# Performance work log

Hardware: AMD Instinct MI355X
Metric: run time of the kernel (lower is better)

Reference implementation:

```python
import jax, jax.numpy as jnp
import numpy as np

B, S, D_MODEL, N_HEADS, HIDDEN = 4, 2048, 1024, 16, 4096
D_HEAD = D_MODEL // N_HEADS
LN_EPS = 1e-5


def setup_inputs() -> dict:
    key = jax.random.key(0)
    ks = jax.random.split(key, 20)
    s = 0.02
    return {
        "X": jax.random.normal(ks[0], (B, S, D_MODEL), dtype=jnp.float32),
        # attention projections (stored [in, out]; y = x @ W + b)
        "Wq": jax.random.normal(ks[1], (D_MODEL, D_MODEL), dtype=jnp.float32) * s,
        "bq": jnp.zeros((D_MODEL,), jnp.float32),
        "Wk": jax.random.normal(ks[2], (D_MODEL, D_MODEL), dtype=jnp.float32) * s,
        "bk": jnp.zeros((D_MODEL,), jnp.float32),
        "Wv": jax.random.normal(ks[3], (D_MODEL, D_MODEL), dtype=jnp.float32) * s,
        "bv": jnp.zeros((D_MODEL,), jnp.float32),
        "Wo": jax.random.normal(ks[4], (D_MODEL, D_MODEL), dtype=jnp.float32) * s,
        "bo": jnp.zeros((D_MODEL,), jnp.float32),
        # layernorm 1
        "g1": jnp.ones((D_MODEL,), jnp.float32),
        "beta1": jnp.zeros((D_MODEL,), jnp.float32),
        # FFN
        "W1": jax.random.normal(ks[5], (D_MODEL, HIDDEN), dtype=jnp.float32) * s,
        "b1": jnp.zeros((HIDDEN,), jnp.float32),
        "W2": jax.random.normal(ks[6], (HIDDEN, D_MODEL), dtype=jnp.float32) * s,
        "b2": jnp.zeros((D_MODEL,), jnp.float32),
        # layernorm 2
        "g2": jnp.ones((D_MODEL,), jnp.float32),
        "beta2": jnp.zeros((D_MODEL,), jnp.float32),
    }


def _layer_norm(x, gamma, beta):
    mu = jnp.mean(x, axis=-1, keepdims=True)
    var = jnp.mean(jnp.square(x - mu), axis=-1, keepdims=True)
    return (x - mu) * jax.lax.rsqrt(var + LN_EPS) * gamma + beta


def reference(X, Wq, bq, Wk, bk, Wv, bv, Wo, bo, g1, beta1, W1, b1, W2, b2, g2, beta2):
    b, s, d = X.shape
    # multi-head attention (dropout is identity in eval mode)
    q = (X @ Wq + bq).reshape(b, s, N_HEADS, D_HEAD)
    k = (X @ Wk + bk).reshape(b, s, N_HEADS, D_HEAD)
    v = (X @ Wv + bv).reshape(b, s, N_HEADS, D_HEAD)
    scale = 1.0 / np.sqrt(D_HEAD).astype(np.float32)
    scores = jnp.einsum('bqhd,bkhd->bhqk', q, k) * scale
    attn = jax.nn.softmax(scores, axis=-1)
    ctx = jnp.einsum('bhqk,bkhd->bqhd', attn, v).reshape(b, s, d)
    attn_out = ctx @ Wo + bo
    # AddNorm 1
    Y = _layer_norm(X + attn_out, g1, beta1)
    # FFN
    ffn_out = jax.nn.relu(Y @ W1 + b1) @ W2 + b2
    # AddNorm 2
    return _layer_norm(Y + ffn_out, g2, beta2)
```

## Files before the change

kernel.cpp:

```cpp
#include <hip/hip_runtime.h>
#include <stdint.h>

typedef unsigned short u16;
typedef short bf16x8 __attribute__((ext_vector_type(8)));
typedef float f32x4 __attribute__((ext_vector_type(4)));
typedef u16 u16x4 __attribute__((ext_vector_type(4)));
typedef u16 u16x8 __attribute__((ext_vector_type(8)));

#define LOG2E 1.4426950408889634f
#define QSCALE (0.125f * LOG2E)

__device__ __forceinline__ u16 f2bf(float f) {
  union { float f; uint32_t u; } x; x.f = f;
  uint32_t r = x.u + 0x7fffu + ((x.u >> 16) & 1u);
  return (u16)(r >> 16);
}
__device__ __forceinline__ u16 f2bf_ru(float f) {
  union { float f; uint32_t u; } x; x.f = f;
  return (u16)((x.u + 0x8000u) >> 16);
}
__device__ __forceinline__ float bf2f(u16 h) {
  union { uint32_t u; float f; } x; x.u = ((uint32_t)h) << 16;
  return x.f;
}
__device__ __forceinline__ uint32_t cvtpk(float lo, float hi) {
  uint32_t r;
  asm("v_cvt_pk_bf16_f32 %0, %1, %2" : "=v"(r) : "v"(lo), "v"(hi));
  return r;
}
__device__ __forceinline__ int swz3(int row) { return (row ^ (row >> 3)) & 7; }

__device__ __forceinline__ void gload_lds16(const void* g, void* lds) {
  __builtin_amdgcn_global_load_lds(
      (const __attribute__((address_space(1))) void*)g,
      (__attribute__((address_space(3))) void*)lds, 16, 0, 0);
}

__global__ __launch_bounds__(256) void cast_bf16(const float* __restrict__ in,
                                                 u16* __restrict__ out, int n8) {
  int i = blockIdx.x * 256 + threadIdx.x;
  const int stride = gridDim.x * 256;
  for (; i < n8; i += stride) {
    const f32x4* p = (const f32x4*)in + (size_t)i * 2;
    f32x4 a = p[0], b = p[1];
    u16x8 o;
    o[0] = f2bf(a[0]); o[1] = f2bf(a[1]); o[2] = f2bf(a[2]); o[3] = f2bf(a[3]);
    o[4] = f2bf(b[0]); o[5] = f2bf(b[1]); o[6] = f2bf(b[2]); o[7] = f2bf(b[3]);
    ((u16x8*)out)[i] = o;
  }
}

__global__ __launch_bounds__(256) void concat3(const float* __restrict__ a,
                                               const float* __restrict__ b,
                                               const float* __restrict__ c,
                                               float* __restrict__ o) {
  int i = blockIdx.x * 256 + threadIdx.x;
  if (i < 3072)
    o[i] = i < 1024 ? a[i] * QSCALE : (i < 2048 ? b[i - 1024] : c[i - 2048]);
}

__global__ __launch_bounds__(256) void transpose_cast(const float* __restrict__ in,
                                                      u16* __restrict__ out, int R, int C,
                                                      float scale) {
  __shared__ float tile[32][33];
  const int bc = blockIdx.x * 32, br = blockIdx.y * 32;
  const int tx = threadIdx.x & 31, ty = threadIdx.x >> 5;
#pragma unroll
  for (int i = 0; i < 32; i += 8)
    tile[ty + i][tx] = in[(size_t)(br + ty + i) * C + bc + tx];
  __syncthreads();
#pragma unroll
  for (int i = 0; i < 32; i += 8)
    out[(size_t)(bc + ty + i) * R + br + tx] = f2bf(tile[tx][ty + i] * scale);
}

__global__ __launch_bounds__(256) void vtrans(const u16* __restrict__ QKV,
                                              u16* __restrict__ Vtg) {
  __shared__ u16 tl[64][65];
  const int t = threadIdx.x;
  const int sblk = blockIdx.x, h = blockIdx.y, b = blockIdx.z;
  const int s0 = sblk * 64;
  const size_t ibase = ((size_t)b * 2048) * 3072 + 2048 + h * 64;
#pragma unroll
  for (int i = 0; i < 2; i++) {
    const int idx = i * 256 + t;
    const int sl = idx >> 3, d0 = (idx & 7) * 8;
    bf16x8 v = *(const bf16x8*)&QKV[ibase + (size_t)(s0 + sl) * 3072 + d0];
#pragma unroll
    for (int e = 0; e < 8; e++) tl[d0 + e][sl] = (u16)v[e];
  }
  __syncthreads();
  const size_t ob = ((size_t)(b * 16 + h) * 64) * 2048;
#pragma unroll
  for (int i = 0; i < 2; i++) {
    const int idx = i * 256 + t;
    const int r = idx >> 3, c0 = (idx & 7) * 8;
    u16x8 o;
#pragma unroll
    for (int e = 0; e < 8; e++) o[e] = tl[r][c0 + e];
    *(u16x8*)&Vtg[ob + (size_t)r * 2048 + s0 + c0] = o;
  }
}

template <int RELU>
__global__ __launch_bounds__(256) void gemm_bt(const u16* __restrict__ A,
                                               const u16* __restrict__ BT,
                                               const float* __restrict__ bias,
                                               u16* __restrict__ Cb,
                                               int M, int N, int K) {
  constexpr int BM = 128, BN = 128, BK = 64;
  __shared__ u16 As[BM * BK];
  __shared__ u16 Bs[BN * BK];
  const int t = threadIdx.x;
  const int w = t >> 6, lane = t & 63;
  const int la = lane & 15, lb = lane >> 4;
  const int wr = w >> 1, wc = w & 1;
  const int m0 = blockIdx.y * BM, n0 = blockIdx.x * BN;

  f32x4 acc[4][4];
#pragma unroll
  for (int i = 0; i < 4; i++)
#pragma unroll
    for (int j = 0; j < 4; j++) acc[i][j] = (f32x4){0.f, 0.f, 0.f, 0.f};

  for (int kt = 0; kt < K; kt += BK) {
#pragma unroll
    for (int i = 0; i < 4; i++) {
      const int s = i * 256 + t;
      const int row = s >> 3, col = (s & 7) * 8;
      gload_lds16(A + (size_t)(m0 + row) * K + kt + col, &As[(i * 256 + w * 64) * 8]);
      gload_lds16(BT + (size_t)(n0 + row) * K + kt + col, &Bs[(i * 256 + w * 64) * 8]);
    }
    __syncthreads();
#pragma unroll
    for (int ks = 0; ks < 2; ks++) {
      bf16x8 af[4], bfr[4];
#pragma unroll
      for (int i = 0; i < 4; i++)
        af[i] = *(const bf16x8*)&As[(wr * 64 + i * 16 + la) * BK + ks * 32 + lb * 8];
#pragma unroll
      for (int j = 0; j < 4; j++)
        bfr[j] = *(const bf16x8*)&Bs[(wc * 64 + j * 16 + la) * BK + ks * 32 + lb * 8];
#pragma unroll
      for (int i = 0; i < 4; i++)
#pragma unroll
        for (int j = 0; j < 4; j++)
          acc[i][j] = __builtin_amdgcn_mfma_f32_16x16x32_bf16(af[i], bfr[j], acc[i][j], 0, 0, 0);
    }
    __syncthreads();
  }
#pragma unroll
  for (int i = 0; i < 4; i++) {
    const int r = m0 + wr * 64 + i * 16 + lb * 4;
#pragma unroll
    for (int j = 0; j < 4; j++) {
      const int c = n0 + wc * 64 + j * 16 + la;
      const float bv = bias[c];
#pragma unroll
      for (int rr = 0; rr < 4; rr++) {
        float v = acc[i][j][rr] + bv;
        if (RELU) v = fmaxf(v, 0.f);
        Cb[(size_t)(r + rr) * N + c] = f2bf(v);
      }
    }
  }
}

template <int RELU>
__global__ __launch_bounds__(512, 2) void gemm8p(const u16* __restrict__ A,
                                                 const u16* __restrict__ BT,
                                                 const float* __restrict__ bias,
                                                 u16* __restrict__ Cb,
                                                 int M, int N, int K, int nbx) {
  __shared__ u16 As[2][256 * 64];
  __shared__ u16 Bs[2][256 * 64];
  const int t = threadIdx.x;
  const int w = t >> 6, lane = t & 63;
  const int la = lane & 15, lb = lane >> 4;
  const int wr = w >> 2, wc = w & 3;
  int bid = (int)blockIdx.x;
  const int cpx = (int)gridDim.x >> 3;
  bid = (bid & 7) * cpx + (bid >> 3);
  const int m0 = (bid / nbx) * 256, n0 = (bid % nbx) * 256;
  const int NT = K >> 6;
  const int row64 = t >> 3;
  const int colp = ((t & 7) ^ swz3(row64)) << 3;

#define STG_A(buf, tile, q) \
  gload_lds16(A + (size_t)(m0 + (q)*64 + row64) * K + ((tile) << 6) + colp, \
              &As[buf][(q)*4096 + w * 512])
#define STG_B(buf, tile, q) \
  gload_lds16(BT + (size_t)(n0 + (q)*64 + row64) * K + ((tile) << 6) + colp, \
              &Bs[buf][(q)*4096 + w * 512])
#define LDA(dst, mf, ks) { const int r_ = wr * 128 + (mf)*16 + la; \
  dst = *(const bf16x8*)&As[cur][r_ * 64 + (((((ks) << 2) + lb) ^ swz3(r_)) << 3)]; }
#define LDB(dst, nf, ks) { const int r_ = wc * 64 + (nf)*16 + la; \
  dst = *(const bf16x8*)&Bs[cur][r_ * 64 + (((((ks) << 2) + lb) ^ swz3(r_)) << 3)]; }
#define MFMA16(mh, nh) \
  __builtin_amdgcn_s_setprio(1); \
  _Pragma("unroll") for (int ks = 0; ks < 2; ks++) \
  _Pragma("unroll") for (int i = 0; i < 4; i++) \
  _Pragma("unroll") for (int j = 0; j < 2; j++) \
    acc[(mh)*4 + i][(nh)*2 + j] = __builtin_amdgcn_mfma_f32_16x16x32_bf16( \
        af[i][ks], bfr[j][ks], acc[(mh)*4 + i][(nh)*2 + j], 0, 0, 0); \
  __builtin_amdgcn_s_setprio(0);
#define BAR1() __builtin_amdgcn_s_barrier(); \
  asm volatile("s_waitcnt lgkmcnt(0)" ::: "memory"); \
  __builtin_amdgcn_sched_barrier(0)

  f32x4 acc[8][4];
#pragma unroll
  for (int i = 0; i < 8; i++)
#pragma unroll
    for (int j = 0; j < 4; j++) acc[i][j] = (f32x4){0.f, 0.f, 0.f, 0.f};

  STG_A(0, 0, 0); STG_A(0, 0, 2);
  STG_B(0, 0, 0); STG_B(0, 0, 1); STG_B(0, 0, 2); STG_B(0, 0, 3);
  STG_A(0, 0, 1); STG_A(0, 0, 3);
  asm volatile("s_waitcnt vmcnt(2)" ::: "memory");
  __builtin_amdgcn_s_barrier();

  for (int tile = 0; tile < NT; ++tile) {
    const int cur = tile & 1, nxt = cur ^ 1;
    const bool hn = (tile + 1) < NT;
    bf16x8 af[4][2], bfr[2][2];
#pragma unroll
    for (int i = 0; i < 4; i++) { LDA(af[i][0], i, 0); LDA(af[i][1], i, 1); }
#pragma unroll
    for (int j = 0; j < 2; j++) { LDB(bfr[j][0], j, 0); LDB(bfr[j][1], j, 1); }
    if (hn) { STG_A(nxt, tile + 1, 0); STG_A(nxt, tile + 1, 2); }
    BAR1();
    MFMA16(0, 0);
    __builtin_amdgcn_s_barrier();
#pragma unroll
    for (int j = 0; j < 2; j++) { LDB(bfr[j][0], 2 + j, 0); LDB(bfr[j][1], 2 + j, 1); }
    if (hn) { STG_B(nxt, tile + 1, 0); STG_B(nxt, tile + 1, 1); }
    BAR1();
    MFMA16(0, 1);
    if (hn) { asm volatile("s_waitcnt vmcnt(4)" ::: "memory"); }
    else    { asm volatile("s_waitcnt vmcnt(0)" ::: "memory"); }
    __builtin_amdgcn_s_barrier();
#pragma unroll
    for (int i = 0; i < 4; i++) { LDA(af[i][0], 4 + i, 0); LDA(af[i][1], 4 + i, 1); }
#pragma unroll
    for (int j = 0; j < 2; j++) { LDB(bfr[j][0], j, 0); LDB(bfr[j][1], j, 1); }
    if (hn) { STG_B(nxt, tile + 1, 2); STG_B(nxt, tile + 1, 3); }
    BAR1();
    MFMA16(1, 0);
    __builtin_amdgcn_s_barrier();
#pragma unroll
    for (int j = 0; j < 2; j++) { LDB(bfr[j][0], 2 + j, 0); LDB(bfr[j][1], 2 + j, 1); }
    if (hn) { STG_A(nxt, tile + 1, 1); STG_A(nxt, tile + 1, 3); }
    BAR1();
    MFMA16(1, 1);
    if (hn) { asm volatile("s_waitcnt vmcnt(2)" ::: "memory"); }
    __builtin_amdgcn_s_barrier();
  }
#undef STG_A
#undef STG_B
#undef LDA
#undef LDB
#undef MFMA16
#undef BAR1

#pragma unroll
  for (int mf = 0; mf < 8; mf++) {
    const int r = m0 + wr * 128 + mf * 16 + lb * 4;
#pragma unroll
    for (int nf = 0; nf < 4; nf++) {
      const int c = n0 + wc * 64 + nf * 16 + la;
      const float bv = bias[c];
#pragma unroll
      for (int rr = 0; rr < 4; rr++) {
        float v = acc[mf][nf][rr] + bv;
        if (RELU) v = fmaxf(v, 0.f);
        Cb[(size_t)(r + rr) * N + c] = f2bf(v);
      }
    }
  }
}

__global__ __launch_bounds__(256) void attn_fwd(const u16* __restrict__ Qg,
                                                const u16* __restrict__ Kg,
                                                const u16* __restrict__ Vtg,
                                                u16* __restrict__ Og, int LDM) {
  constexpr int S = 2048, DMO = 1024;
  __shared__ u16 Ks[2][128 * 64];
  __shared__ u16 Vt[2][64 * 128];
  const int t = threadIdx.x, w = t >> 6, lane = t & 63;
  const int la = lane & 15, lb = lane >> 4;
  const int qb = blockIdx.x, h = blockIdx.y, b = blockIdx.z;
  const size_t base = ((size_t)b * S) * LDM + h * 64;
  const size_t vbase = ((size_t)(b * 16 + h) * 64) * 2048;
  const size_t obase = ((size_t)b * S) * DMO + h * 64;
  const int qrow0 = qb * 128 + w * 32;
  const int sl0 = la + 32 * (lb & 1), sl1 = sl0 + 16;
  const int jsel = lb >> 1;

#define ATT_STAGE(buf, kt_) { \
  _Pragma("unroll") for (int i = 0; i < 4; i++) { \
    const int s = i * 256 + t; const int r = s >> 3; const int cg = s & 7; \
    gload_lds16(Kg + base + (size_t)((kt_) + r) * LDM + ((cg ^ swz3(r)) << 3), \
                &Ks[buf][s * 8]); } \
  _Pragma("unroll") for (int i = 0; i < 4; i++) { \
    const int s = i * 256 + t; const int r = s >> 4; const int cg = s & 15; \
    gload_lds16(Vtg + vbase + (size_t)r * 2048 + (kt_) + ((cg ^ swz3(r)) << 3), \
                &Vt[buf][s * 8]); } }

  bf16x8 qf[2][2];
#pragma unroll
  for (int rf = 0; rf < 2; rf++)
#pragma unroll
    for (int ks = 0; ks < 2; ks++)
      qf[rf][ks] = *(const bf16x8*)&Qg[base + (size_t)(qrow0 + rf * 16 + la) * LDM + ks * 32 + lb * 8];

  f32x4 accO[2][4];
  float m[2], l[2];
#pragma unroll
  for (int i = 0; i < 2; i++) {
    m[i] = -1e30f; l[i] = 0.f;
#pragma unroll
    for (int j = 0; j < 4; j++) accO[i][j] = (f32x4){0.f, 0.f, 0.f, 0.f};
  }

  ATT_STAGE(0, 0);
  asm volatile("s_waitcnt vmcnt(0)" ::: "memory");
  __builtin_amdgcn_s_barrier();

  for (int kt2 = 0; kt2 < S / 128; ++kt2) {
    const int cur = kt2 & 1;
    if (kt2 + 1 < S / 128) ATT_STAGE(cur ^ 1, (kt2 + 1) * 128);

#pragma unroll
    for (int sub = 0; sub < 2; ++sub) {
      f32x4 st[4][2];
#pragma unroll
      for (int j = 0; j < 4; j++)
#pragma unroll
        for (int rf = 0; rf < 2; rf++) st[j][rf] = (f32x4){0.f, 0.f, 0.f, 0.f};
      __builtin_amdgcn_s_setprio(1);
#pragma unroll
      for (int ks = 0; ks < 2; ks++) {
        bf16x8 kf[4];
#pragma unroll
        for (int j = 0; j < 4; j++) {
          const int r = sub * 64 + j * 16 + la;
          kf[j] = *(const bf16x8*)&Ks[cur][r * 64 + ((((ks << 2) + lb) ^ swz3(r)) << 3)];
        }
#pragma unroll
        for (int j = 0; j < 4; j++)
#pragma unroll
          for (int rf = 0; rf < 2; rf++)
            st[j][rf] = __builtin_amdgcn_mfma_f32_16x16x32_bf16(kf[j], qf[rf][ks], st[j][rf], 0, 0, 0);
      }
      __builtin_amdgcn_s_setprio(0);

      bf16x8 pf[2][2];
#pragma unroll
      for (int rf = 0; rf < 2; rf++) {
        float rm = st[0][rf][0];
#pragma unroll
        for (int j = 0; j < 4; j++)
#pragma unroll
          for (int rr = 0; rr < 4; rr++) rm = fmaxf(rm, st[j][rf][rr]);
        if (__any(rm > m[rf] + 8.0f)) {
          rm = fmaxf(rm, __shfl_xor(rm, 16, 64));
          rm = fmaxf(rm, __shfl_xor(rm, 32, 64));
          const float mN = fmaxf(m[rf], rm);
          const float al = exp2f(m[rf] - mN);
          m[rf] = mN;
          l[rf] *= al;
#pragma unroll
          for (int rr = 0; rr < 4; rr++) {
            const float alr = __shfl(al, (lb << 2) + rr, 64);
#pragma unroll
            for (int cf = 0; cf < 4; cf++) accO[rf][cf][rr] *= alr;
          }
        }
        uint32_t wl[4], wh[4];
#pragma unroll
        for (int j = 0; j < 4; j++) {
          float p0 = exp2f(st[j][rf][0] - m[rf]);
          float p1 = exp2f(st[j][rf][1] - m[rf]);
          float p2 = exp2f(st[j][rf][2] - m[rf]);
          float p3 = exp2f(st[j][rf][3] - m[rf]);
          l[rf] += (p0 + p1) + (p2 + p3);
          wl[j] = cvtpk(p0, p1);
          wh[j] = cvtpk(p2, p3);
        }
#pragma unroll
        for (int ks = 0; ks < 2; ks++) {
          const int j0 = 2 * ks, j1 = 2 * ks + 1;
          uint32_t a0 = __shfl(wl[j0], sl0, 64), a1 = __shfl(wh[j0], sl0, 64);
          uint32_t a2 = __shfl(wl[j0], sl1, 64), a3 = __shfl(wh[j0], sl1, 64);
          uint32_t b0 = __shfl(wl[j1], sl0, 64), b1 = __shfl(wh[j1], sl0, 64);
          uint32_t b2 = __shfl(wl[j1], sl1, 64), b3 = __shfl(wh[j1], sl1, 64);
          union { uint32_t u[4]; bf16x8 v; } pk;
          pk.u[0] = jsel ? b0 : a0;
          pk.u[1] = jsel ? b1 : a1;
          pk.u[2] = jsel ? b2 : a2;
          pk.u[3] = jsel ? b3 : a3;
          pf[rf][ks] = pk.v;
        }
      }

      __builtin_amdgcn_s_setprio(1);
#pragma unroll
      for (int ks = 0; ks < 2; ks++) {
        bf16x8 vf[4];
#pragma unroll
        for (int cf = 0; cf < 4; cf++) {
          const int dr = cf * 16 + la;
          const int g = sub * 8 + ks * 4 + lb;
          vf[cf] = *(const bf16x8*)&Vt[cur][dr * 128 + ((g ^ swz3(dr)) << 3)];
        }
#pragma unroll
        for (int rf = 0; rf < 2; rf++)
#pragma unroll
          for (int cf = 0; cf < 4; cf++)
            accO[rf][cf] = __builtin_amdgcn_mfma_f32_16x16x32_bf16(pf[rf][ks], vf[cf], accO[rf][cf], 0, 0, 0);
      }
      __builtin_amdgcn_s_setprio(0);
    }

    asm volatile("s_waitcnt vmcnt(0)" ::: "memory");
    __builtin_amdgcn_s_barrier();
  }
#undef ATT_STAGE

#pragma unroll
  for (int rf = 0; rf < 2; rf++) {
    float l2 = l[rf];
    l2 += __shfl_xor(l2, 16, 64);
    l2 += __shfl_xor(l2, 32, 64);
    const float inv = 1.0f / l2;
#pragma unroll
    for (int rr = 0; rr < 4; rr++) {
      const float invr = __shfl(inv, (lb << 2) + rr, 64);
      const int r = qrow0 + rf * 16 + lb * 4 + rr;
#pragma unroll
      for (int cf = 0; cf < 4; cf++)
        Og[obase + (size_t)r * DMO + cf * 16 + la] = f2bf_ru(accO[rf][cf][rr] * invr);
    }
  }
}

template <int AF32, int OUTF32>
__global__ __launch_bounds__(256) void add_ln(const void* __restrict__ Ap,
                                              const u16* __restrict__ Bb,
                                              const float* __restrict__ g,
                                              const float* __restrict__ be,
                                              void* __restrict__ Yp) {
  constexpr int D = 1024;
  const int row = blockIdx.x, t = threadIdx.x;
  f32x4 a;
  if (AF32) {
    a = ((const f32x4*)((const float*)Ap + (size_t)row * D))[t];
  } else {
    u16x4 av = ((const u16x4*)((const u16*)Ap + (size_t)row * D))[t];
#pragma unroll
    for (int i = 0; i < 4; i++) a[i] = bf2f(av[i]);
  }
  u16x4 bv16 = ((const u16x4*)(Bb + (size_t)row * D))[t];
  f32x4 x;
#pragma unroll
  for (int i = 0; i < 4; i++) x[i] = a[i] + bf2f(bv16[i]);
  float s1 = x[0] + x[1] + x[2] + x[3];
  float s2 = x[0] * x[0] + x[1] * x[1] + x[2] * x[2] + x[3] * x[3];
#pragma unroll
  for (int off = 32; off > 0; off >>= 1) {
    s1 += __shfl_down(s1, off, 64);
    s2 += __shfl_down(s2, off, 64);
  }
  __shared__ float sm[8];
  const int w = t >> 6, lane = t & 63;
  if (lane == 0) { sm[w] = s1; sm[4 + w] = s2; }
  __syncthreads();
  s1 = sm[0] + sm[1] + sm[2] + sm[3];
  s2 = sm[4] + sm[5] + sm[6] + sm[7];
  const float mean = s1 * (1.0f / D);
  const float var = s2 * (1.0f / D) - mean * mean;
  const float rstd = rsqrtf(var + 1e-5f);
  const f32x4 gv = ((const f32x4*)g)[t];
  const f32x4 bv = ((const f32x4*)be)[t];
  f32x4 y;
#pragma unroll
  for (int i = 0; i < 4; i++) y[i] = (x[i] - mean) * rstd * gv[i] + bv[i];
  if (OUTF32) {
    ((f32x4*)((float*)Yp + (size_t)row * D))[t] = y;
  } else {
    u16x4 o;
#pragma unroll
    for (int i = 0; i < 4; i++) o[i] = f2bf(y[i]);
    ((u16x4*)((u16*)Yp + (size_t)row * D))[t] = o;
  }
}

extern "C" void kernel_launch(void* const* d_in, const int* in_sizes, int n_in,
                              void* d_out, int out_size, void* d_ws, size_t ws_size,
                              hipStream_t stream) {
  const float* X   = (const float*)d_in[0];
  const float* Wq  = (const float*)d_in[1];
  const float* bq  = (const float*)d_in[2];
  const float* Wk  = (const float*)d_in[3];
  const float* bk  = (const float*)d_in[4];
  const float* Wv  = (const float*)d_in[5];
  const float* bv  = (const float*)d_in[6];
  const float* Wo  = (const float*)d_in[7];
  const float* bo  = (const float*)d_in[8];
  const float* g1  = (const float*)d_in[9];
  const float* be1 = (const float*)d_in[10];
  const float* W1  = (const float*)d_in[11];
  const float* b1  = (const float*)d_in[12];
  const float* W2  = (const float*)d_in[13];
  const float* b2  = (const float*)d_in[14];
  const float* g2  = (const float*)d_in[15];
  const float* be2 = (const float*)d_in[16];

  const size_t MB = 1ull << 20;
  char* wsb = (char*)d_ws;
  u16*   WqkvT = (u16*)(wsb + 0 * MB);
  u16*   WoT   = (u16*)(wsb + 6 * MB);
  u16*   W1T   = (u16*)(wsb + 8 * MB);
  u16*   W2T   = (u16*)(wsb + 16 * MB);
  u16*   Xb    = (u16*)(wsb + 24 * MB);
  u16*   Ab    = (u16*)(wsb + 24 * MB);
  u16*   Fb    = (u16*)(wsb + 24 * MB);
  u16*   QKVb  = (u16*)(wsb + 40 * MB);
  u16*   Hb    = (u16*)(wsb + 40 * MB);
  float* bqkv  = (float*)(wsb + 88 * MB);
  u16*   Cx    = (u16*)(wsb + 88 * MB);
  u16*   Vt_g  = (u16*)(wsb + 104 * MB);
  u16*   Yb    = (u16*)(wsb + 104 * MB);
  (void)ws_size; (void)in_sizes; (void)n_in; (void)out_size;

  cast_bf16<<<2048, 256, 0, stream>>>(X, Xb, 8192 * 1024 / 8);
  concat3<<<12, 256, 0, stream>>>(bq, bk, bv, bqkv);
  transpose_cast<<<dim3(32, 32), 256, 0, stream>>>(Wq, WqkvT, 1024, 1024, QSCALE);
  transpose_cast<<<dim3(32, 32), 256, 0, stream>>>(Wk, WqkvT + 1024 * 1024, 1024, 1024, 1.0f);
  transpose_cast<<<dim3(32, 32), 256, 0, stream>>>(Wv, WqkvT + 2 * 1024 * 1024, 1024, 1024, 1.0f);
  transpose_cast<<<dim3(32, 32), 256, 0, stream>>>(Wo, WoT, 1024, 1024, 1.0f);
  transpose_cast<<<dim3(128, 32), 256, 0, stream>>>(W1, W1T, 1024, 4096, 1.0f);
  transpose_cast<<<dim3(32, 128), 256, 0, stream>>>(W2, W2T, 4096, 1024, 1.0f);

  gemm8p<0><<<32 * 12, 512, 0, stream>>>(Xb, WqkvT, bqkv, QKVb, 8192, 3072, 1024, 12);

  vtrans<<<dim3(32, 16, 4), 256, 0, stream>>>(QKVb, Vt_g);
  attn_fwd<<<dim3(16, 16, 4), 256, 0, stream>>>(QKVb, QKVb + 1024, Vt_g, Cx, 3072);

  gemm_bt<0><<<dim3(8, 64), 256, 0, stream>>>(Cx, WoT, bo, Ab, 8192, 1024, 1024);
  add_ln<1, 0><<<8192, 256, 0, stream>>>(X, Ab, g1, be1, Yb);
  gemm8p<1><<<32 * 16, 512, 0, stream>>>(Yb, W1T, b1, Hb, 8192, 4096, 1024, 16);
  gemm_bt<0><<<dim3(8, 64), 256, 0, stream>>>(Hb, W2T, b2, Fb, 8192, 1024, 4096);
  add_ln<0, 1><<<8192, 256, 0, stream>>>(Yb, Fb, g2, be2, d_out);
}
```

Measured before the change: 502.8 us.

## Replace simple GEMM with double-buffered swizzled 256x128 pipelined GEMM kernel

Replaces the single-buffered 128x128 gemm_bt with a new 512-thread, double-buffered 256x128-tile GEMM. It uses XOR-swizzled LDS, split-phase prefetch with vmcnt waits, setprio around the MFMA blocks, and a block-index remap for L2 locality. The new kernel serves the Wo and W2 projections and also the QKV projection in place of gemm8p with 256x256 tiles. The aim is to overlap global loads with MFMA work and remove LDS bank conflicts. In exchange, the smaller N tile on QKV lowers data reuse, and the 256x128 tiles give only 256 blocks for the N=1024 GEMMs, which may limit occupancy.

```diff
diff --git a/kernel.cpp b/kernel.cpp
--- a/kernel.cpp
+++ b/kernel.cpp
@@ -103,62 +103,99 @@
 }
 
 template <int RELU>
-__global__ __launch_bounds__(256) void gemm_bt(const u16* __restrict__ A,
-                                               const u16* __restrict__ BT,
-                                               const float* __restrict__ bias,
-                                               u16* __restrict__ Cb,
-                                               int M, int N, int K) {
-  constexpr int BM = 128, BN = 128, BK = 64;
-  __shared__ u16 As[BM * BK];
-  __shared__ u16 Bs[BN * BK];
+__global__ __launch_bounds__(512, 2) void gemm2p(const u16* __restrict__ A,
+                                                 const u16* __restrict__ BT,
+                                                 const float* __restrict__ bias,
+                                                 u16* __restrict__ Cb,
+                                                 int M, int N, int K, int nbx) {
+  __shared__ u16 As[2][256 * 64];
+  __shared__ u16 Bs[2][128 * 64];
   const int t = threadIdx.x;
   const int w = t >> 6, lane = t & 63;
   const int la = lane & 15, lb = lane >> 4;
-  const int wr = w >> 1, wc = w & 1;
-  const int m0 = blockIdx.y * BM, n0 = blockIdx.x * BN;
-
-  f32x4 acc[4][4];
-#pragma unroll
-  for (int i = 0; i < 4; i++)
-#pragma unroll
-    for (int j = 0; j < 4; j++) acc[i][j] = (f32x4){0.f, 0.f, 0.f, 0.f};
-
-  for (int kt = 0; kt < K; kt += BK) {
-#pragma unroll
-    for (int i = 0; i < 4; i++) {
-      const int s = i * 256 + t;
-      const int row = s >> 3, col = (s & 7) * 8;
-      gload_lds16(A + (size_t)(m0 + row) * K + kt + col, &As[(i * 256 + w * 64) * 8]);
-      gload_lds16(BT + (size_t)(n0 + row) * K + kt + col, &Bs[(i * 256 + w * 64) * 8]);
-    }
-    __syncthreads();
-#pragma unroll
-    for (int ks = 0; ks < 2; ks++) {
-      bf16x8 af[4], bfr[4];
-#pragma unroll
-      for (int i = 0; i < 4; i++)
-        af[i] = *(const bf16x8*)&As[(wr * 64 + i * 16 + la) * BK + ks * 32 + lb * 8];
-#pragma unroll
-      for (int j = 0; j < 4; j++)
-        bfr[j] = *(const bf16x8*)&Bs[(wc * 64 + j * 16 + la) * BK + ks * 32 + lb * 8];
-#pragma unroll
-      for (int i = 0; i < 4; i++)
-#pragma unroll
-        for (int j = 0; j < 4; j++)
-          acc[i][j] = __builtin_amdgcn_mfma_f32_16x16x32_bf16(af[i], bfr[j], acc[i][j], 0, 0, 0);
-    }
-    __syncthreads();
-  }
-#pragma unroll
-  for (int i = 0; i < 4; i++) {
-    const int r = m0 + wr * 64 + i * 16 + lb * 4;
-#pragma unroll
-    for (int j = 0; j < 4; j++) {
-      const int c = n0 + wc * 64 + j * 16 + la;
+  const int wr = w >> 2, wc = w & 3;
+  int bid = (int)blockIdx.x;
+  const int cpx = (int)gridDim.x >> 3;
+  bid = (bid & 7) * cpx + (bid >> 3);
+  const int m0 = (bid / nbx) * 256, n0 = (bid % nbx) * 128;
+  const int NT = K >> 6;
+  const int row64 = t >> 3;
+  const int colp = ((t & 7) ^ swz3(row64)) << 3;
+
+#define STG_A2(buf, tile, q) \
+  gload_lds16(A + (size_t)(m0 + (q)*64 + row64) * K + ((tile) << 6) + colp, \
+              &As[buf][(q)*4096 + w * 512])
+#define STG_B2(buf, tile, h) \
+  gload_lds16(BT + (size_t)(n0 + (h)*64 + row64) * K + ((tile) << 6) + colp, \
+              &Bs[buf][(h)*4096 + w * 512])
+#define LDA2(dst, mf, ks) { const int r_ = wr * 128 + (mf)*16 + la; \
+  dst = *(const bf16x8*)&As[cur][r_ * 64 + (((((ks) << 2) + lb) ^ swz3(r_)) << 3)]; }
+#define LDB2(dst, nf, ks) { const int r_ = wc * 32 + (nf)*16 + la; \
+  dst = *(const bf16x8*)&Bs[cur][r_ * 64 + (((((ks) << 2) + lb) ^ swz3(r_)) << 3)]; }
+#define MFMA2(mh) \
+  __builtin_amdgcn_s_setprio(1); \
+  _Pragma("unroll") for (int ks = 0; ks < 2; ks++) \
+  _Pragma("unroll") for (int i = 0; i < 4; i++) \
+  _Pragma("unroll") for (int j = 0; j < 2; j++) \
+    acc[(mh)*4 + i][j] = __builtin_amdgcn_mfma_f32_16x16x32_bf16( \
+        af[i][ks], bfr[j][ks], acc[(mh)*4 + i][j], 0, 0, 0); \
+  __builtin_amdgcn_s_setprio(0);
+#define BAR2() __builtin_amdgcn_s_barrier(); \
+  asm volatile("s_waitcnt lgkmcnt(0)" ::: "memory"); \
+  __builtin_amdgcn_sched_barrier(0)
+
+  f32x4 acc[8][2];
+#pragma unroll
+  for (int i = 0; i < 8; i++)
+#pragma unroll
+    for (int j = 0; j < 2; j++) acc[i][j] = (f32x4){0.f, 0.f, 0.f, 0.f};
+
+  STG_A2(0, 0, 0); STG_A2(0, 0, 2); STG_B2(0, 0, 0); STG_B2(0, 0, 1);
+  STG_A2(0, 0, 1); STG_A2(0, 0, 3);
+  asm volatile("s_waitcnt vmcnt(0)" ::: "memory");
+  __builtin_amdgcn_s_barrier();
+
+  for (int tile = 0; tile < NT; ++tile) {
+    const int cur = tile & 1, nxt = cur ^ 1;
+    const bool hn = (tile + 1) < NT;
+    bf16x8 af[4][2], bfr[2][2];
+#pragma unroll
+    for (int i = 0; i < 4; i++) { LDA2(af[i][0], i, 0); LDA2(af[i][1], i, 1); }
+#pragma unroll
+    for (int j = 0; j < 2; j++) { LDB2(bfr[j][0], j, 0); LDB2(bfr[j][1], j, 1); }
+    if (hn) { STG_A2(nxt, tile + 1, 0); STG_A2(nxt, tile + 1, 2); STG_B2(nxt, tile + 1, 0); }
+    BAR2();
+    MFMA2(0);
+    if (hn) { asm volatile("s_waitcnt vmcnt(3)" ::: "memory"); }
+    else    { asm volatile("s_waitcnt vmcnt(0)" ::: "memory"); }
+    __builtin_amdgcn_s_barrier();
+#pragma unroll
+    for (int i = 0; i < 4; i++) { LDA2(af[i][0], 4 + i, 0); LDA2(af[i][1], 4 + i, 1); }
+#pragma unroll
+    for (int j = 0; j < 2; j++) { LDB2(bfr[j][0], j, 0); LDB2(bfr[j][1], j, 1); }
+    if (hn) { STG_B2(nxt, tile + 1, 1); STG_A2(nxt, tile + 1, 1); STG_A2(nxt, tile + 1, 3); }
+    BAR2();
+    MFMA2(1);
+    if (hn) { asm volatile("s_waitcnt vmcnt(2)" ::: "memory"); }
+    __builtin_amdgcn_s_barrier();
+  }
+#undef STG_A2
+#undef STG_B2
+#undef LDA2
+#undef LDB2
+#undef MFMA2
+#undef BAR2
+
+#pragma unroll
+  for (int mf = 0; mf < 8; mf++) {
+    const int r = m0 + wr * 128 + mf * 16 + lb * 4;
+#pragma unroll
+    for (int nf = 0; nf < 2; nf++) {
+      const int c = n0 + wc * 32 + nf * 16 + la;
       const float bv = bias[c];
 #pragma unroll
       for (int rr = 0; rr < 4; rr++) {
-        float v = acc[i][j][rr] + bv;
+        float v = acc[mf][nf][rr] + bv;
         if (RELU) v = fmaxf(v, 0.f);
         Cb[(size_t)(r + rr) * N + c] = f2bf(v);
       }
@@ -543,14 +580,14 @@
   transpose_cast<<<dim3(128, 32), 256, 0, stream>>>(W1, W1T, 1024, 4096, 1.0f);
   transpose_cast<<<dim3(32, 128), 256, 0, stream>>>(W2, W2T, 4096, 1024, 1.0f);
 
-  gemm8p<0><<<32 * 12, 512, 0, stream>>>(Xb, WqkvT, bqkv, QKVb, 8192, 3072, 1024, 12);
+  gemm2p<0><<<768, 512, 0, stream>>>(Xb, WqkvT, bqkv, QKVb, 8192, 3072, 1024, 24);
 
   vtrans<<<dim3(32, 16, 4), 256, 0, stream>>>(QKVb, Vt_g);
   attn_fwd<<<dim3(16, 16, 4), 256, 0, stream>>>(QKVb, QKVb + 1024, Vt_g, Cx, 3072);
 
-  gemm_bt<0><<<dim3(8, 64), 256, 0, stream>>>(Cx, WoT, bo, Ab, 8192, 1024, 1024);
+  gemm2p<0><<<256, 512, 0, stream>>>(Cx, WoT, bo, Ab, 8192, 1024, 1024, 8);
   add_ln<1, 0><<<8192, 256, 0, stream>>>(X, Ab, g1, be1, Yb);
-  gemm8p<1><<<32 * 16, 512, 0, stream>>>(Yb, W1T, b1, Hb, 8192, 4096, 1024, 16);
-  gemm_bt<0><<<dim3(8, 64), 256, 0, stream>>>(Hb, W2T, b2, Fb, 8192, 1024, 4096);
+  gemm8p<1><<<512, 512, 0, stream>>>(Yb, W1T, b1, Hb, 8192, 4096, 1024, 16);
+  gemm2p<0><<<256, 512, 0, stream>>>(Hb, W2T, b2, Fb, 8192, 1024, 4096, 8);
   add_ln<0, 1><<<8192, 256, 0, stream>>>(Yb, Fb, g2, be2, d_out);
 }
```

Measured after the change: 511.8 us. No clear change (+1.8%).
